# Performance work log

Hardware: AMD Instinct MI355X
Metric: run time of the kernel (lower is better)

Reference implementation:

```python
import jax, jax.numpy as jnp
import numpy as np

N, E = 50000, 200000
SIZES = [16, 32, 16]
EDIM = 8
EPS = 1e-5


def setup_inputs() -> dict:
    key = jax.random.key(0)
    ks = jax.random.split(key, 16)
    inp = {
        "x": jax.random.normal(ks[0], (N, SIZES[0]), jnp.float32),
        "edge_attr": jax.random.normal(ks[1], (E, EDIM), jnp.float32),
        "edge_index": jax.random.randint(ks[2], (2, E), 0, N, dtype=jnp.int32),
    }
    ki = 3
    for l in range(2):
        fin, fout = SIZES[l], SIZES[l + 1]
        m = fin * fout
        # xavier-ish init matching torch.nn.init.xavier_uniform_ scales
        inp[f"W1_{l}"] = jax.random.normal(ks[ki], (EDIM, m), jnp.float32) / np.float32(np.sqrt(EDIM)); ki += 1
        inp[f"b1_{l}"] = jnp.zeros((m,), jnp.float32)
        inp[f"W2_{l}"] = jax.random.normal(ks[ki], (m, m), jnp.float32) * np.float32(0.01 / np.sqrt(m)); ki += 1
        inp[f"b2_{l}"] = jnp.zeros((m,), jnp.float32)
        inp[f"root_{l}"] = jax.random.normal(ks[ki], (fin, fout), jnp.float32) / np.float32(np.sqrt(fin)); ki += 1
        inp[f"bias_{l}"] = jnp.zeros((fout,), jnp.float32)
        inp[f"gamma_{l}"] = jnp.ones((fout,), jnp.float32)
        inp[f"beta_{l}"] = jnp.zeros((fout,), jnp.float32)
    return inp


def _lrelu(v):
    return jnp.where(v >= 0, v, 0.01 * v)


def _nnconv(x, src, dst, edge_attr, W1, b1, W2, b2, root, bias, fin, fout):
    # edge MLP -> per-edge weight matrix [E, fin, fout]
    h = _lrelu(edge_attr @ W1 + b1) @ W2 + b2
    h = h.reshape(-1, fin, fout)
    # gather source node features, tiny per-edge matmul
    msg = jnp.einsum('ei,eio->eo', x[src], h)  # [E, fout]
    # scatter-mean aggregate at destination nodes
    agg = jax.ops.segment_sum(msg, dst, num_segments=N)
    deg = jax.ops.segment_sum(jnp.ones((msg.shape[0],), msg.dtype), dst, num_segments=N)
    agg = agg / jnp.maximum(deg, 1.0)[:, None]
    return agg + x @ root + bias


def _bn(v, gamma, beta):
    # BatchNorm1d (training mode: batch stats, biased variance)
    mu = v.mean(0)
    var = v.var(0)
    return (v - mu) * jax.lax.rsqrt(var + EPS) * gamma + beta


def reference(x, edge_attr,
              W1_0, b1_0, W2_0, b2_0, root_0, bias_0, gamma_0, beta_0,
              W1_1, b1_1, W2_1, b2_1, root_1, bias_1, gamma_1, beta_1,
              edge_index):
    src, dst = edge_index[0], edge_index[1]
    h = _nnconv(x, src, dst, edge_attr, W1_0, b1_0, W2_0, b2_0, root_0, bias_0, SIZES[0], SIZES[1])
    h = _lrelu(_bn(h, gamma_0, beta_0))
    h = _nnconv(h, src, dst, edge_attr, W1_1, b1_1, W2_1, b2_1, root_1, bias_1, SIZES[1], SIZES[2])
    return _bn(h, gamma_1, beta_1)
```

## Files before the change

### kernel.cpp

```cpp
#include <hip/hip_runtime.h>
#include <hip/hip_bf16.h>

typedef __attribute__((ext_vector_type(4))) float f32x4;
typedef __attribute__((ext_vector_type(8))) short s16x8;
typedef __attribute__((ext_vector_type(4))) int int4v;

#define DEVI __device__ __forceinline__

constexpr int NN = 50000;
constexpr int NE = 200000;
constexpr float BN_EPS = 1e-5f;

DEVI float bfbits2f(unsigned v) { union { unsigned u; float f; } t; t.u = v << 16; return t.f; }
DEVI float lrelu_f(float v) { return v >= 0.f ? v : 0.01f * v; }

__global__ void k_transpose_w2(const float* __restrict__ A0, const float* __restrict__ A1,
                               __hip_bfloat16* __restrict__ T0, __hip_bfloat16* __restrict__ T1) {
  const float* W2 = blockIdx.y ? A1 : A0;
  __hip_bfloat16* W2T = blockIdx.y ? T1 : T0;
  __shared__ float tile[32][33];
  int bx = blockIdx.x % 16, by = blockIdx.x / 16;
  int t = threadIdx.x;
  int r = t / 32, c = t % 32;
  for (int rr = r; rr < 32; rr += 8)
    tile[rr][c] = W2[(size_t)(by * 32 + rr) * 512 + bx * 32 + c];
  __syncthreads();
  for (int rr = r; rr < 32; rr += 8)
    W2T[(size_t)(bx * 32 + rr) * 512 + by * 32 + c] = __float2bfloat16(tile[c][rr]);
}

__global__ void k_transpose_w1(const float* __restrict__ A0, const float* __restrict__ A1,
                               __hip_bfloat16* __restrict__ T0, __hip_bfloat16* __restrict__ T1) {
  const float* W1 = blockIdx.y ? A1 : A0;
  __hip_bfloat16* W1T = blockIdx.y ? T1 : T0;
  int tid = blockIdx.x * 256 + threadIdx.x;
  if (tid < 8 * 512) {
    int k = tid / 512, n = tid % 512;
    W1T[n * 8 + k] = __float2bfloat16(W1[tid]);
  }
}

__global__ void k_count(const int* __restrict__ dst, int* __restrict__ cnt) {
  int e = blockIdx.x * 256 + threadIdx.x;
  if (e < NE) atomicAdd(&cnt[dst[e]], 1);
}

constexpr int SCAN_ELEMS = 1024;
__global__ void k_scan1(const int* __restrict__ cnt, int* __restrict__ base, int* __restrict__ aux, int n) {
  __shared__ int sw[256];
  int b = blockIdx.x, t = threadIdx.x;
  int i0 = b * SCAN_ELEMS + t * 4;
  int v[4]; int s = 0;
  #pragma unroll
  for (int j = 0; j < 4; j++) { int idx = i0 + j; v[j] = (idx < n) ? cnt[idx] : 0; s += v[j]; }
  sw[t] = s; __syncthreads();
  for (int d = 1; d < 256; d <<= 1) {
    int val = (t >= d) ? sw[t - d] : 0;
    __syncthreads();
    sw[t] += val;
    __syncthreads();
  }
  int run = (t > 0) ? sw[t - 1] : 0;
  #pragma unroll
  for (int j = 0; j < 4; j++) { int idx = i0 + j; if (idx < n) base[idx] = run; run += v[j]; }
  if (t == 255) aux[b] = sw[255];
}

__global__ void k_scan2(int* aux, int nb) {
  if (threadIdx.x == 0 && blockIdx.x == 0) {
    int run = 0;
    for (int i = 0; i < nb; i++) { int v = aux[i]; aux[i] = run; run += v; }
  }
}

__global__ void k_scan3(int* __restrict__ base, int* __restrict__ cursor, const int* __restrict__ aux, int n) {
  int i = blockIdx.x * 256 + threadIdx.x;
  if (i < n) { int v = base[i] + aux[i / SCAN_ELEMS]; base[i] = v; cursor[i] = v; }
}

__global__ void k_place(const int* __restrict__ dst, int* __restrict__ cursor, int* __restrict__ perm) {
  int e = blockIdx.x * 256 + threadIdx.x;
  if (e < NE) { int p = atomicAdd(&cursor[dst[e]], 1); perm[p] = e; }
}

template <int FIN, int FOUT>
__global__ __launch_bounds__(256, 3)
void k_edge(const float* __restrict__ x, const float* __restrict__ ea,
            const int* __restrict__ srcI,
            const __hip_bfloat16* __restrict__ W1T, const float* __restrict__ b1,
            const __hip_bfloat16* __restrict__ W2T, const float* __restrict__ b2,
            __hip_bfloat16* __restrict__ msgb)
{
  static_assert(FOUT == 32 || FOUT == 16, "");
  constexpr int TM = 256;
  constexpr int CG = 32;
  constexpr int NCGI = 16;
  constexpr int KH = 128;
  constexpr int NSW = 4;
  constexpr int NOT = FOUT / 16;
  constexpr int XLDS = TM + 8;

  __shared__ __align__(16) char bbuf[2][CG * 256];
  __shared__ __align__(16) char gbuf[4][4096];
  __shared__ __align__(16) __hip_bfloat16 xlt[FIN][XLDS];

  const int tid = threadIdx.x;
  const int lane = tid & 63, w = tid >> 6;
  const int l15 = lane & 15, l4 = lane >> 4;
  const int e0 = blockIdx.x * TM;
  const int rem = min(TM, NE - e0);
  const int wrow0 = w * 64;

  union { s16x8 v; int i4[4]; } earow;
  {
    int er = e0 + min(tid, rem - 1);
    float4 v0 = *(const float4*)(ea + (size_t)er * 8);
    float4 v1 = *(const float4*)(ea + (size_t)er * 8 + 4);
    __hip_bfloat16* p = (__hip_bfloat16*)&earow;
    p[0] = __float2bfloat16(v0.x); p[1] = __float2bfloat16(v0.y);
    p[2] = __float2bfloat16(v0.z); p[3] = __float2bfloat16(v0.w);
    p[4] = __float2bfloat16(v1.x); p[5] = __float2bfloat16(v1.y);
    p[6] = __float2bfloat16(v1.z); p[7] = __float2bfloat16(v1.w);
    int s = srcI[er];
    #pragma unroll
    for (int q = 0; q < FIN / 4; q++) {
      float4 xv4 = *(const float4*)(x + (size_t)s * FIN + q * 4);
      xlt[q * 4 + 0][tid] = __float2bfloat16(xv4.x);
      xlt[q * 4 + 1][tid] = __float2bfloat16(xv4.y);
      xlt[q * 4 + 2][tid] = __float2bfloat16(xv4.z);
      xlt[q * 4 + 3][tid] = __float2bfloat16(xv4.w);
    }
  }

  f32x4 msg[4][NOT];
  #pragma unroll
  for (int rt = 0; rt < 4; rt++)
    #pragma unroll
    for (int ot = 0; ot < NOT; ot++) msg[rt][ot] = (f32x4)(0.f);

  s16x8 af[4][4];
  const int st_col = tid >> 3, st_s = tid & 7;
  const char* W2Tb = (const char*)W2T;
  char* gme = gbuf[w];
  int4v sr0, sr1;

  for (int sw = 0; sw < NSW; ++sw) {
    {
      const char* gp = W2Tb + (size_t)st_col * 1024 + sw * 256;
      sr0 = *(const int4v*)(gp + st_s * 16);
      sr1 = *(const int4v*)(gp + (st_s + 8) * 16);
    }
    #pragma unroll
    for (int hr = 0; hr < 2; ++hr) {
      s16x8 afe[2];
      #pragma unroll
      for (int rt2 = 0; rt2 < 2; rt2++) {
        union { s16x8 v; int i4[4]; } t2;
        #pragma unroll
        for (int q = 0; q < 4; q++) t2.i4[q] = __shfl(earow.i4[q], (hr * 2 + rt2) * 16 + l15);
        afe[rt2] = (lane < 16) ? t2.v : (s16x8)0;
      }
      #pragma unroll
      for (int hk = 0; hk < 2; ++hk) {
        #pragma unroll
        for (int ct = 0; ct < 4; ct++) {
          int c = sw * KH + hk * 64 + ct * 16 + l15;
          s16x8 bw = *(const s16x8*)(W1T + c * 8);
          bw = (lane < 16) ? bw : (s16x8)0;
          float b1v = b1[c];
          #pragma unroll
          for (int rt2 = 0; rt2 < 2; rt2++) {
            f32x4 d = __builtin_amdgcn_mfma_f32_16x16x32_bf16(afe[rt2], bw, (f32x4)(0.f), 0, 0, 0);
            #pragma unroll
            for (int r = 0; r < 4; r++) {
              int rloc = rt2 * 16 + l4 * 4 + r;
              float gv = d[r] + b1v;
              gv = gv >= 0.f ? gv : 0.01f * gv;
              int byt = (rloc * 128 + (ct * 16 + l15) * 2) ^ ((rloc & 7) << 4);
              *(__hip_bfloat16*)(gme + byt) = __float2bfloat16(gv);
            }
          }
        }
        #pragma unroll
        for (int rt2 = 0; rt2 < 2; rt2++)
          #pragma unroll
          for (int kk = 0; kk < 2; kk++) {
            int rloc = rt2 * 16 + l15;
            int byt = (rloc * 128 + (kk * 32 + l4 * 8) * 2) ^ ((rloc & 7) << 4);
            af[hk * 2 + kk][hr * 2 + rt2] = *(const s16x8*)(gme + byt);
          }
      }
    }
    #pragma unroll
    for (int kst = 0; kst < 4; kst++)
      #pragma unroll
      for (int rt = 0; rt < 4; rt++)
        asm volatile("" : "+v"(af[kst][rt]));

    *(int4v*)(&bbuf[0][st_col * 256 + ((st_s ^ (st_col & 7)) << 4)]) = sr0;
    *(int4v*)(&bbuf[0][st_col * 256 + (((st_s + 8) ^ (st_col & 7)) << 4)]) = sr1;
    __syncthreads();

    for (int cgi = 0; cgi < NCGI; ++cgi) {
      if (cgi + 1 < NCGI) {
        const char* gp = W2Tb + (size_t)((cgi + 1) * CG + st_col) * 1024 + sw * 256;
        sr0 = *(const int4v*)(gp + st_s * 16);
        sr1 = *(const int4v*)(gp + (st_s + 8) * 16);
      }
      const char* bb = bbuf[cgi & 1];

      #pragma unroll
      for (int ct = 0; ct < 2; ++ct) {
        const int c = ct * 16 + l15;
        const int cbase = c * 256;
        const int csw = c & 7;
        f32x4 acc[4];
        if (sw == 0) {
          float b2v = b2[cgi * CG + c];
          acc[0] = (f32x4)(b2v); acc[1] = (f32x4)(b2v);
          acc[2] = (f32x4)(b2v); acc[3] = (f32x4)(b2v);
        } else {
          acc[0] = (f32x4)(0.f); acc[1] = (f32x4)(0.f);
          acc[2] = (f32x4)(0.f); acc[3] = (f32x4)(0.f);
        }
        #pragma unroll
        for (int kst = 0; kst < 4; ++kst) {
          const int slot = kst * 4 + l4;
          const s16x8 bw = *(const s16x8*)(bb + cbase + ((slot ^ csw) << 4));
          #pragma unroll
          for (int rt = 0; rt < 4; rt++)
            acc[rt] = __builtin_amdgcn_mfma_f32_16x16x32_bf16(af[kst][rt], bw, acc[rt], 0, 0, 0);
        }
        const int iv = (FOUT == 32) ? cgi : (cgi * 2 + ct);
        const int ot = (FOUT == 32) ? ct : 0;
        #pragma unroll
        for (int rt = 0; rt < 4; rt++) {
          int rbase = wrow0 + rt * 16 + l4 * 4;
          ushort4 xv = *(const ushort4*)(&xlt[iv][rbase]);
          msg[rt][ot][0] += bfbits2f(xv.x) * acc[rt][0];
          msg[rt][ot][1] += bfbits2f(xv.y) * acc[rt][1];
          msg[rt][ot][2] += bfbits2f(xv.z) * acc[rt][2];
          msg[rt][ot][3] += bfbits2f(xv.w) * acc[rt][3];
        }
      }
      if (cgi + 1 < NCGI) {
        char* bw2 = bbuf[(cgi + 1) & 1];
        *(int4v*)(&bw2[st_col * 256 + ((st_s ^ (st_col & 7)) << 4)]) = sr0;
        *(int4v*)(&bw2[st_col * 256 + (((st_s + 8) ^ (st_col & 7)) << 4)]) = sr1;
      }
      __syncthreads();
    }
  }

  #pragma unroll
  for (int rt = 0; rt < 4; rt++)
    #pragma unroll
    for (int r = 0; r < 4; r++) {
      int row = wrow0 + rt * 16 + l4 * 4 + r;
      if (row < rem) {
        #pragma unroll
        for (int ot = 0; ot < NOT; ot++)
          msgb[(size_t)(e0 + row) * FOUT + ot * 16 + l15] = __float2bfloat16(msg[rt][ot][r]);
      }
    }
}

template <int FIN, int FOUT>
__global__ void k_node_agg(const __hip_bfloat16* __restrict__ msgb, const int* __restrict__ perm,
                           const int* __restrict__ base,
                           const float* __restrict__ x,
                           const float* __restrict__ root,
                           const float* __restrict__ bias,
                           float* __restrict__ h)
{
  __shared__ float rl[FIN * FOUT];
  constexpr int NPB = 256 / FOUT;
  int t = threadIdx.x;
  for (int i = t; i < FIN * FOUT; i += 256) rl[i] = root[i];
  __syncthreads();
  int n = blockIdx.x * NPB + t / FOUT;
  int o = t % FOUT;
  if (n >= NN) return;
  int s = base[n];
  int e = (n + 1 < NN) ? base[n + 1] : NE;
  float sum = 0.f;
  for (int j = s; j < e; j++)
    sum += __bfloat162float(msgb[(size_t)perm[j] * FOUT + o]);
  float acc = sum / fmaxf((float)(e - s), 1.f) + bias[o];
  #pragma unroll
  for (int i = 0; i < FIN; i++)
    acc += x[(size_t)n * FIN + i] * rl[i * FOUT + o];
  h[(size_t)n * FOUT + o] = acc;
}

template <int FOUT>
__global__ void k_stats(const float* __restrict__ h, float* __restrict__ ssum, float* __restrict__ ssq) {
  constexpr int RPB = 256 / FOUT;
  int t = threadIdx.x;
  int o = t % FOUT, rr = t / FOUT;
  float v = 0.f, v2 = 0.f;
  for (int r = blockIdx.x * RPB + rr; r < NN; r += gridDim.x * RPB) {
    float y = h[(size_t)r * FOUT + o];
    v += y; v2 += y * y;
  }
  #pragma unroll
  for (int d = FOUT; d < 64; d <<= 1) { v += __shfl_xor(v, d); v2 += __shfl_xor(v2, d); }
  __shared__ float sv[4][32], sq[4][32];
  int wv = t >> 6, ln = t & 63;
  if (ln < FOUT) { sv[wv][ln] = v; sq[wv][ln] = v2; }
  __syncthreads();
  if (t < FOUT) {
    float a = 0.f, b = 0.f;
    #pragma unroll
    for (int w2 = 0; w2 < 4; w2++) { a += sv[w2][t]; b += sq[w2][t]; }
    atomicAdd(&ssum[t], a);
    atomicAdd(&ssq[t], b);
  }
}

template <int FOUT, bool LRELU>
__global__ void k_bn(const float* __restrict__ h, const float* __restrict__ ssum,
                     const float* __restrict__ ssq, const float* __restrict__ gamma,
                     const float* __restrict__ beta, float* __restrict__ out)
{
  int idx = blockIdx.x * 256 + threadIdx.x;
  if (idx * 4 >= NN * FOUT) return;
  float4 v = *(const float4*)(h + (size_t)idx * 4);
  float r[4] = {v.x, v.y, v.z, v.w};
  #pragma unroll
  for (int j = 0; j < 4; j++) {
    int o = (idx * 4 + j) % FOUT;
    float mu = ssum[o] * (1.f / NN);
    float var = ssq[o] * (1.f / NN) - mu * mu;
    float sc = rsqrtf(var + BN_EPS) * gamma[o];
    float y = (r[j] - mu) * sc + beta[o];
    if (LRELU) y = lrelu_f(y);
    r[j] = y;
  }
  *(float4*)(out + (size_t)idx * 4) = make_float4(r[0], r[1], r[2], r[3]);
}

extern "C" void kernel_launch(void* const* d_in, const int* in_sizes, int n_in,
                              void* d_out, int out_size, void* d_ws, size_t ws_size,
                              hipStream_t stream)
{
  const float* x0    = (const float*)d_in[0];
  const float* ea    = (const float*)d_in[1];
  const int*   ei    = (const int*)d_in[2];
  const float* W1_0  = (const float*)d_in[3];
  const float* b1_0  = (const float*)d_in[4];
  const float* W2_0  = (const float*)d_in[5];
  const float* b2_0  = (const float*)d_in[6];
  const float* root0 = (const float*)d_in[7];
  const float* bias0 = (const float*)d_in[8];
  const float* gam0  = (const float*)d_in[9];
  const float* bet0  = (const float*)d_in[10];
  const float* W1_1  = (const float*)d_in[11];
  const float* b1_1  = (const float*)d_in[12];
  const float* W2_1  = (const float*)d_in[13];
  const float* b2_1  = (const float*)d_in[14];
  const float* root1 = (const float*)d_in[15];
  const float* bias1 = (const float*)d_in[16];
  const float* gam1  = (const float*)d_in[17];
  const float* bet1  = (const float*)d_in[18];
  const int* srcI = ei;
  const int* dstI = ei + NE;

  char* ws = (char*)d_ws;
  size_t off = 0;
  auto alloc = [&](size_t bytes) { char* p = ws + off; off += (bytes + 255) & ~(size_t)255; return p; };
  int*   cnt   = (int*)alloc(50048 * 4);
  float* ssum0 = (float*)alloc(32 * 4);
  float* ssq0  = (float*)alloc(32 * 4);
  float* ssum1 = (float*)alloc(16 * 4);
  float* ssq1  = (float*)alloc(16 * 4);
  size_t zero_bytes = off;
  int*   base   = (int*)alloc(50048 * 4);
  int*   cursor = (int*)alloc(50048 * 4);
  int*   aux    = (int*)alloc(64 * 4);
  int*   perm   = (int*)alloc((size_t)NE * 4);
  __hip_bfloat16* msgb = (__hip_bfloat16*)alloc((size_t)NE * 32 * 2);
  float* h0 = (float*)alloc((size_t)NN * 32 * 4);
  float* h1 = (float*)alloc((size_t)NN * 16 * 4);
  float* x1 = (float*)alloc((size_t)NN * 32 * 4);
  __hip_bfloat16* W2T0 = (__hip_bfloat16*)alloc(512 * 512 * 2);
  __hip_bfloat16* W2T1 = (__hip_bfloat16*)alloc(512 * 512 * 2);
  __hip_bfloat16* W1T0 = (__hip_bfloat16*)alloc(512 * 8 * 2);
  __hip_bfloat16* W1T1 = (__hip_bfloat16*)alloc(512 * 8 * 2);

  hipMemsetAsync(d_ws, 0, zero_bytes, stream);

  k_transpose_w2<<<dim3(256, 2), 256, 0, stream>>>(W2_0, W2_1, W2T0, W2T1);
  k_transpose_w1<<<dim3(16, 2), 256, 0, stream>>>(W1_0, W1_1, W1T0, W1T1);

  constexpr int NSB = (NN + SCAN_ELEMS - 1) / SCAN_ELEMS;
  k_count<<<(NE + 255) / 256, 256, 0, stream>>>(dstI, cnt);
  k_scan1<<<NSB, 256, 0, stream>>>(cnt, base, aux, NN);
  k_scan2<<<1, 64, 0, stream>>>(aux, NSB);
  k_scan3<<<(NN + 255) / 256, 256, 0, stream>>>(base, cursor, aux, NN);
  k_place<<<(NE + 255) / 256, 256, 0, stream>>>(dstI, cursor, perm);

  constexpr int TM = 256;
  k_edge<16, 32><<<(NE + TM - 1) / TM, 256, 0, stream>>>(x0, ea, srcI, W1T0, b1_0, W2T0, b2_0, msgb);
  k_node_agg<16, 32><<<(NN + 7) / 8, 256, 0, stream>>>(msgb, perm, base, x0, root0, bias0, h0);
  k_stats<32><<<128, 256, 0, stream>>>(h0, ssum0, ssq0);
  k_bn<32, true><<<((NN * 32 / 4) + 255) / 256, 256, 0, stream>>>(h0, ssum0, ssq0, gam0, bet0, x1);

  k_edge<32, 16><<<(NE + TM - 1) / TM, 256, 0, stream>>>(x1, ea, srcI, W1T1, b1_1, W2T1, b2_1, msgb);
  k_node_agg<32, 16><<<(NN + 15) / 16, 256, 0, stream>>>(msgb, perm, base, x1, root1, bias1, h1);
  k_stats<16><<<128, 256, 0, stream>>>(h1, ssum1, ssq1);
  k_bn<16, false><<<((NN * 16 / 4) + 255) / 256, 256, 0, stream>>>(h1, ssum1, ssq1, gam1, bet1, (float*)d_out);
}
```

Baseline: 484.8 us.

## Stage whole W2 K-slice in LDS via direct global-to-LDS loads with 512-edge tiles

The edge kernel now processes 512 edges per 512-thread block and loads the entire per-sweep W2 K-slice (all 512 or 448 columns) into shared memory with global_load_lds, instead of double-buffering 32-column chunks through registers with a barrier per chunk. This removes the 16 per-chunk syncthreads per sweep and halves the number of W2 re-reads from L2. The tail columns that overlap the edge-MLP scratch are loaded after that stage and guarded by one extra barrier. For the FIN=32 layer, which has less LDS room, the last columns are read directly from global memory. The larger LDS footprint and block size may reduce occupancy, and the direct global reads in the tail may add latency.

```diff
diff --git a/kernel.cpp b/kernel.cpp
--- a/kernel.cpp
+++ b/kernel.cpp
@@ -6,6 +6,10 @@
 typedef __attribute__((ext_vector_type(4))) int int4v;
 
 #define DEVI __device__ __forceinline__
+
+#define GLL16(gp, lp) __builtin_amdgcn_global_load_lds( \
+    (const __attribute__((address_space(1))) void*)(gp), \
+    (__attribute__((address_space(3))) void*)(lp), 16, 0, 0)
 
 constexpr int NN = 50000;
 constexpr int NE = 200000;
@@ -84,7 +88,7 @@
 }
 
 template <int FIN, int FOUT>
-__global__ __launch_bounds__(256, 3)
+__global__ __launch_bounds__(512, 2)
 void k_edge(const float* __restrict__ x, const float* __restrict__ ea,
             const int* __restrict__ srcI,
             const __hip_bfloat16* __restrict__ W1T, const float* __restrict__ b1,
@@ -92,17 +96,19 @@
             __hip_bfloat16* __restrict__ msgb)
 {
   static_assert(FOUT == 32 || FOUT == 16, "");
-  constexpr int TM = 256;
-  constexpr int CG = 32;
-  constexpr int NCGI = 16;
-  constexpr int KH = 128;
-  constexpr int NSW = 4;
+  constexpr int TM = 512;
+  constexpr int KH = 128, NSW = 4;
   constexpr int NOT = FOUT / 16;
-  constexpr int XLDS = TM + 8;
-
-  __shared__ __align__(16) char bbuf[2][CG * 256];
-  __shared__ __align__(16) char gbuf[4][4096];
-  __shared__ __align__(16) __hip_bfloat16 xlt[FIN][XLDS];
+  constexpr int PCOLS = (FIN == 16) ? 512 : 448;
+  constexpr int NCGL = PCOLS / 32;
+  constexpr int CGC = (PCOLS - 128) / 32;
+  constexpr int MAINB = PCOLS * 256;
+  constexpr int GOFF = MAINB - 32768;
+  constexpr int NQE = (PCOLS - 128) / 4;
+  constexpr int QPW = NQE / 8;
+
+  __shared__ __align__(16) char main_[MAINB];
+  __shared__ __align__(16) __hip_bfloat16 xlt[FIN][TM];
 
   const int tid = threadIdx.x;
   const int lane = tid & 63, w = tid >> 6;
@@ -139,17 +145,19 @@
     for (int ot = 0; ot < NOT; ot++) msg[rt][ot] = (f32x4)(0.f);
 
   s16x8 af[4][4];
-  const int st_col = tid >> 3, st_s = tid & 7;
   const char* W2Tb = (const char*)W2T;
-  char* gme = gbuf[w];
-  int4v sr0, sr1;
+  char* gme = main_ + GOFF + w * 4096;
 
   for (int sw = 0; sw < NSW; ++sw) {
-    {
-      const char* gp = W2Tb + (size_t)st_col * 1024 + sw * 256;
-      sr0 = *(const int4v*)(gp + st_s * 16);
-      sr1 = *(const int4v*)(gp + (st_s + 8) * 16);
-    }
+    __syncthreads();
+    #pragma unroll
+    for (int t = 0; t < QPW; ++t) {
+      int colq = w * QPW + t;
+      int col = colq * 4 + (lane >> 4);
+      int ssrc = (lane & 15) ^ (col & 7);
+      GLL16(W2Tb + (size_t)col * 1024 + sw * 256 + (size_t)ssrc * 16, main_ + colq * 1024);
+    }
+
     #pragma unroll
     for (int hr = 0; hr < 2; ++hr) {
       s16x8 afe[2];
@@ -197,41 +205,34 @@
       for (int rt = 0; rt < 4; rt++)
         asm volatile("" : "+v"(af[kst][rt]));
 
-    *(int4v*)(&bbuf[0][st_col * 256 + ((st_s ^ (st_col & 7)) << 4)]) = sr0;
-    *(int4v*)(&bbuf[0][st_col * 256 + (((st_s + 8) ^ (st_col & 7)) << 4)]) = sr1;
     __syncthreads();
 
-    for (int cgi = 0; cgi < NCGI; ++cgi) {
-      if (cgi + 1 < NCGI) {
-        const char* gp = W2Tb + (size_t)((cgi + 1) * CG + st_col) * 1024 + sw * 256;
-        sr0 = *(const int4v*)(gp + st_s * 16);
-        sr1 = *(const int4v*)(gp + (st_s + 8) * 16);
-      }
-      const char* bb = bbuf[cgi & 1];
-
+    #pragma unroll
+    for (int t = 0; t < 4; ++t) {
+      int colq = NQE + w * 4 + t;
+      int col = colq * 4 + (lane >> 4);
+      int ssrc = (lane & 15) ^ (col & 7);
+      GLL16(W2Tb + (size_t)col * 1024 + sw * 256 + (size_t)ssrc * 16, main_ + colq * 1024);
+    }
+
+    for (int cgi = 0; cgi < NCGL; ++cgi) {
+      if (cgi == CGC) __syncthreads();
       #pragma unroll
       for (int ct = 0; ct < 2; ++ct) {
-        const int c = ct * 16 + l15;
-        const int cbase = c * 256;
-        const int csw = c & 7;
+        const int c = cgi * 32 + ct * 16 + l15;
         f32x4 acc[4];
-        if (sw == 0) {
-          float b2v = b2[cgi * CG + c];
-          acc[0] = (f32x4)(b2v); acc[1] = (f32x4)(b2v);
-          acc[2] = (f32x4)(b2v); acc[3] = (f32x4)(b2v);
-        } else {
-          acc[0] = (f32x4)(0.f); acc[1] = (f32x4)(0.f);
-          acc[2] = (f32x4)(0.f); acc[3] = (f32x4)(0.f);
-        }
+        float ai = (sw == 0) ? b2[c] : 0.f;
+        acc[0] = (f32x4)(ai); acc[1] = (f32x4)(ai);
+        acc[2] = (f32x4)(ai); acc[3] = (f32x4)(ai);
+        const int cbase = c * 256, csw = c & 7;
         #pragma unroll
         for (int kst = 0; kst < 4; ++kst) {
-          const int slot = kst * 4 + l4;
-          const s16x8 bw = *(const s16x8*)(bb + cbase + ((slot ^ csw) << 4));
+          const s16x8 bw = *(const s16x8*)(main_ + cbase + (((kst * 4 + l4) ^ csw) << 4));
           #pragma unroll
           for (int rt = 0; rt < 4; rt++)
             acc[rt] = __builtin_amdgcn_mfma_f32_16x16x32_bf16(af[kst][rt], bw, acc[rt], 0, 0, 0);
         }
-        const int iv = (FOUT == 32) ? cgi : (cgi * 2 + ct);
+        const int iv = (FOUT == 32) ? (c >> 5) : (c >> 4);
         const int ot = (FOUT == 32) ? ct : 0;
         #pragma unroll
         for (int rt = 0; rt < 4; rt++) {
@@ -243,12 +244,36 @@
           msg[rt][ot][3] += bfbits2f(xv.w) * acc[rt][3];
         }
       }
-      if (cgi + 1 < NCGI) {
-        char* bw2 = bbuf[(cgi + 1) & 1];
-        *(int4v*)(&bw2[st_col * 256 + ((st_s ^ (st_col & 7)) << 4)]) = sr0;
-        *(int4v*)(&bw2[st_col * 256 + (((st_s + 8) ^ (st_col & 7)) << 4)]) = sr1;
+    }
+    if constexpr (PCOLS < 512) {
+      for (int cgi = NCGL; cgi < 16; ++cgi) {
+        #pragma unroll
+        for (int ct = 0; ct < 2; ++ct) {
+          const int c = cgi * 32 + ct * 16 + l15;
+          f32x4 acc[4];
+          float ai = (sw == 0) ? b2[c] : 0.f;
+          acc[0] = (f32x4)(ai); acc[1] = (f32x4)(ai);
+          acc[2] = (f32x4)(ai); acc[3] = (f32x4)(ai);
+          #pragma unroll
+          for (int kst = 0; kst < 4; ++kst) {
+            const s16x8 bw = *(const s16x8*)(W2Tb + (size_t)c * 1024 + sw * 256 + (kst * 4 + l4) * 16);
+            #pragma unroll
+            for (int rt = 0; rt < 4; rt++)
+              acc[rt] = __builtin_amdgcn_mfma_f32_16x16x32_bf16(af[kst][rt], bw, acc[rt], 0, 0, 0);
+          }
+          const int iv = (FOUT == 32) ? (c >> 5) : (c >> 4);
+          const int ot = (FOUT == 32) ? ct : 0;
+          #pragma unroll
+          for (int rt = 0; rt < 4; rt++) {
+            int rbase = wrow0 + rt * 16 + l4 * 4;
+            ushort4 xv = *(const ushort4*)(&xlt[iv][rbase]);
+            msg[rt][ot][0] += bfbits2f(xv.x) * acc[rt][0];
+            msg[rt][ot][1] += bfbits2f(xv.y) * acc[rt][1];
+            msg[rt][ot][2] += bfbits2f(xv.z) * acc[rt][2];
+            msg[rt][ot][3] += bfbits2f(xv.w) * acc[rt][3];
+          }
+        }
       }
-      __syncthreads();
     }
   }
 
@@ -400,13 +425,13 @@
   k_scan3<<<(NN + 255) / 256, 256, 0, stream>>>(base, cursor, aux, NN);
   k_place<<<(NE + 255) / 256, 256, 0, stream>>>(dstI, cursor, perm);
 
-  constexpr int TM = 256;
-  k_edge<16, 32><<<(NE + TM - 1) / TM, 256, 0, stream>>>(x0, ea, srcI, W1T0, b1_0, W2T0, b2_0, msgb);
+  constexpr int TM = 512;
+  k_edge<16, 32><<<(NE + TM - 1) / TM, 512, 0, stream>>>(x0, ea, srcI, W1T0, b1_0, W2T0, b2_0, msgb);
   k_node_agg<16, 32><<<(NN + 7) / 8, 256, 0, stream>>>(msgb, perm, base, x0, root0, bias0, h0);
   k_stats<32><<<128, 256, 0, stream>>>(h0, ssum0, ssq0);
   k_bn<32, true><<<((NN * 32 / 4) + 255) / 256, 256, 0, stream>>>(h0, ssum0, ssq0, gam0, bet0, x1);
 
-  k_edge<32, 16><<<(NE + TM - 1) / TM, 256, 0, stream>>>(x1, ea, srcI, W1T1, b1_1, W2T1, b2_1, msgb);
+  k_edge<32, 16><<<(NE + TM - 1) / TM, 512, 0, stream>>>(x1, ea, srcI, W1T1, b1_1, W2T1, b2_1, msgb);
   k_node_agg<32, 16><<<(NN + 15) / 16, 256, 0, stream>>>(msgb, perm, base, x1, root1, bias1, h1);
   k_stats<16><<<128, 256, 0, stream>>>(h1, ssum1, ssq1);
   k_bn<16, false><<<((NN * 16 / 4) + 255) / 256, 256, 0, stream>>>(h1, ssum1, ssq1, gam1, bet1, (float*)d_out);
```

Measured after the change: 455.4 us. 1.06x faster.

## Switch edge kernel to 32x32x16 MFMA with 512-edge tiles and 256-wide K chunks

Applied to the files above, without the earlier changes.

Rewrites the per-edge MLP kernel to use 32x32x16 bf16 MFMA tiles instead of 16x16x32, doubles the edge tile to 512 with 512-thread blocks, and halves the number of K sweeps over W2 by staging 256-wide chunks. The aim is to raise MFMA efficiency per shared-memory B-fragment load and to reload W2 fewer times per edge. In exchange it holds many more A fragments in registers (16x2 s16x8), which raises register pressure and may cut occupancy. It also adds a shuffle reduction for the FOUT=16 output.

```diff
diff --git a/kernel.cpp b/kernel.cpp
--- a/kernel.cpp
+++ b/kernel.cpp
@@ -2,6 +2,7 @@
 #include <hip/hip_bf16.h>
 
 typedef __attribute__((ext_vector_type(4))) float f32x4;
+typedef __attribute__((ext_vector_type(16))) float f32x16;
 typedef __attribute__((ext_vector_type(8))) short s16x8;
 typedef __attribute__((ext_vector_type(4))) int int4v;
 
@@ -84,7 +85,7 @@
 }
 
 template <int FIN, int FOUT>
-__global__ __launch_bounds__(256, 3)
+__global__ __launch_bounds__(512, 2)
 void k_edge(const float* __restrict__ x, const float* __restrict__ ea,
             const int* __restrict__ srcI,
             const __hip_bfloat16* __restrict__ W1T, const float* __restrict__ b1,
@@ -92,21 +93,20 @@
             __hip_bfloat16* __restrict__ msgb)
 {
   static_assert(FOUT == 32 || FOUT == 16, "");
-  constexpr int TM = 256;
+  constexpr int TM = 512;
   constexpr int CG = 32;
   constexpr int NCGI = 16;
-  constexpr int KH = 128;
-  constexpr int NSW = 4;
-  constexpr int NOT = FOUT / 16;
+  constexpr int KH = 256;
+  constexpr int NSW = 2;
   constexpr int XLDS = TM + 8;
 
-  __shared__ __align__(16) char bbuf[2][CG * 256];
-  __shared__ __align__(16) char gbuf[4][4096];
+  __shared__ __align__(16) char bbuf[2][CG * 512];
+  __shared__ __align__(16) char gbuf[8][4096];
   __shared__ __align__(16) __hip_bfloat16 xlt[FIN][XLDS];
 
   const int tid = threadIdx.x;
   const int lane = tid & 63, w = tid >> 6;
-  const int l15 = lane & 15, l4 = lane >> 4;
+  const int l31 = lane & 31, lhi = lane >> 5;
   const int e0 = blockIdx.x * TM;
   const int rem = min(TM, NE - e0);
   const int wrow0 = w * 64;
@@ -132,137 +132,131 @@
     }
   }
 
-  f32x4 msg[4][NOT];
-  #pragma unroll
-  for (int rt = 0; rt < 4; rt++)
-    #pragma unroll
-    for (int ot = 0; ot < NOT; ot++) msg[rt][ot] = (f32x4)(0.f);
-
-  s16x8 af[4][4];
-  const int st_col = tid >> 3, st_s = tid & 7;
+  f32x16 msg0 = (f32x16)(0.f), msg1 = (f32x16)(0.f);
+  s16x8 af[16][2];
+  const int st_col = tid >> 4, st_s = tid & 15;
   const char* W2Tb = (const char*)W2T;
   char* gme = gbuf[w];
   int4v sr0, sr1;
 
   for (int sw = 0; sw < NSW; ++sw) {
     {
-      const char* gp = W2Tb + (size_t)st_col * 1024 + sw * 256;
+      const char* gp = W2Tb + (size_t)st_col * 1024 + sw * 512;
       sr0 = *(const int4v*)(gp + st_s * 16);
-      sr1 = *(const int4v*)(gp + (st_s + 8) * 16);
-    }
-    #pragma unroll
-    for (int hr = 0; hr < 2; ++hr) {
-      s16x8 afe[2];
-      #pragma unroll
-      for (int rt2 = 0; rt2 < 2; rt2++) {
+      sr1 = *(const int4v*)(gp + (st_s + 16) * 16);
+    }
+    #pragma unroll
+    for (int tile = 0; tile < 2; ++tile) {
+      s16x8 ae;
+      {
         union { s16x8 v; int i4[4]; } t2;
         #pragma unroll
-        for (int q = 0; q < 4; q++) t2.i4[q] = __shfl(earow.i4[q], (hr * 2 + rt2) * 16 + l15);
-        afe[rt2] = (lane < 16) ? t2.v : (s16x8)0;
-      }
-      #pragma unroll
-      for (int hk = 0; hk < 2; ++hk) {
+        for (int q = 0; q < 4; q++) t2.i4[q] = __shfl(earow.i4[q], tile * 32 + l31);
+        ae = (lane < 32) ? t2.v : (s16x8)0;
+      }
+      #pragma unroll
+      for (int chunk = 0; chunk < 4; ++chunk) {
         #pragma unroll
-        for (int ct = 0; ct < 4; ct++) {
-          int c = sw * KH + hk * 64 + ct * 16 + l15;
-          s16x8 bw = *(const s16x8*)(W1T + c * 8);
-          bw = (lane < 16) ? bw : (s16x8)0;
-          float b1v = b1[c];
+        for (int ctile = 0; ctile < 2; ++ctile) {
+          int gcolg = sw * KH + chunk * 64 + ctile * 32 + l31;
+          s16x8 bw = (s16x8)0;
+          if (lane < 32) bw = *(const s16x8*)(W1T + gcolg * 8);
+          float b1v = b1[gcolg];
+          f32x16 d = __builtin_amdgcn_mfma_f32_32x32x16_bf16(ae, bw, (f32x16)(0.f), 0, 0, 0);
           #pragma unroll
-          for (int rt2 = 0; rt2 < 2; rt2++) {
-            f32x4 d = __builtin_amdgcn_mfma_f32_16x16x32_bf16(afe[rt2], bw, (f32x4)(0.f), 0, 0, 0);
-            #pragma unroll
-            for (int r = 0; r < 4; r++) {
-              int rloc = rt2 * 16 + l4 * 4 + r;
-              float gv = d[r] + b1v;
-              gv = gv >= 0.f ? gv : 0.01f * gv;
-              int byt = (rloc * 128 + (ct * 16 + l15) * 2) ^ ((rloc & 7) << 4);
-              *(__hip_bfloat16*)(gme + byt) = __float2bfloat16(gv);
-            }
+          for (int r = 0; r < 16; r++) {
+            int rowloc = (r & 3) + 8 * (r >> 2) + 4 * lhi;
+            float gv = d[r] + b1v;
+            gv = gv >= 0.f ? gv : 0.01f * gv;
+            int gcl = ctile * 32 + l31;
+            int byt = (rowloc * 128 + gcl * 2) ^ ((rowloc & 7) << 4);
+            *(__hip_bfloat16*)(gme + byt) = __float2bfloat16(gv);
           }
         }
         #pragma unroll
-        for (int rt2 = 0; rt2 < 2; rt2++)
-          #pragma unroll
-          for (int kk = 0; kk < 2; kk++) {
-            int rloc = rt2 * 16 + l15;
-            int byt = (rloc * 128 + (kk * 32 + l4 * 8) * 2) ^ ((rloc & 7) << 4);
-            af[hk * 2 + kk][hr * 2 + rt2] = *(const s16x8*)(gme + byt);
-          }
-      }
-    }
-    #pragma unroll
-    for (int kst = 0; kst < 4; kst++)
-      #pragma unroll
-      for (int rt = 0; rt < 4; rt++)
-        asm volatile("" : "+v"(af[kst][rt]));
-
-    *(int4v*)(&bbuf[0][st_col * 256 + ((st_s ^ (st_col & 7)) << 4)]) = sr0;
-    *(int4v*)(&bbuf[0][st_col * 256 + (((st_s + 8) ^ (st_col & 7)) << 4)]) = sr1;
+        for (int kk = 0; kk < 4; ++kk) {
+          int byt = (l31 * 128 + (kk * 16 + lhi * 8) * 2) ^ ((l31 & 7) << 4);
+          af[chunk * 4 + kk][tile] = *(const s16x8*)(gme + byt);
+        }
+      }
+    }
+    #pragma unroll
+    for (int kst = 0; kst < 16; kst++)
+      #pragma unroll
+      for (int tile = 0; tile < 2; tile++)
+        asm volatile("" : "+v"(af[kst][tile]));
+
+    *(int4v*)(&bbuf[0][st_col * 512 + ((st_s ^ (st_col & 7)) << 4)]) = sr0;
+    *(int4v*)(&bbuf[0][st_col * 512 + (((st_s + 16) ^ (st_col & 7)) << 4)]) = sr1;
     __syncthreads();
 
     for (int cgi = 0; cgi < NCGI; ++cgi) {
       if (cgi + 1 < NCGI) {
-        const char* gp = W2Tb + (size_t)((cgi + 1) * CG + st_col) * 1024 + sw * 256;
+        const char* gp = W2Tb + (size_t)((cgi + 1) * CG + st_col) * 1024 + sw * 512;
         sr0 = *(const int4v*)(gp + st_s * 16);
-        sr1 = *(const int4v*)(gp + (st_s + 8) * 16);
+        sr1 = *(const int4v*)(gp + (st_s + 16) * 16);
       }
       const char* bb = bbuf[cgi & 1];
-
-      #pragma unroll
-      for (int ct = 0; ct < 2; ++ct) {
-        const int c = ct * 16 + l15;
-        const int cbase = c * 256;
-        const int csw = c & 7;
-        f32x4 acc[4];
-        if (sw == 0) {
-          float b2v = b2[cgi * CG + c];
-          acc[0] = (f32x4)(b2v); acc[1] = (f32x4)(b2v);
-          acc[2] = (f32x4)(b2v); acc[3] = (f32x4)(b2v);
-        } else {
-          acc[0] = (f32x4)(0.f); acc[1] = (f32x4)(0.f);
-          acc[2] = (f32x4)(0.f); acc[3] = (f32x4)(0.f);
-        }
-        #pragma unroll
-        for (int kst = 0; kst < 4; ++kst) {
-          const int slot = kst * 4 + l4;
-          const s16x8 bw = *(const s16x8*)(bb + cbase + ((slot ^ csw) << 4));
-          #pragma unroll
-          for (int rt = 0; rt < 4; rt++)
-            acc[rt] = __builtin_amdgcn_mfma_f32_16x16x32_bf16(af[kst][rt], bw, acc[rt], 0, 0, 0);
-        }
-        const int iv = (FOUT == 32) ? cgi : (cgi * 2 + ct);
-        const int ot = (FOUT == 32) ? ct : 0;
-        #pragma unroll
-        for (int rt = 0; rt < 4; rt++) {
-          int rbase = wrow0 + rt * 16 + l4 * 4;
-          ushort4 xv = *(const ushort4*)(&xlt[iv][rbase]);
-          msg[rt][ot][0] += bfbits2f(xv.x) * acc[rt][0];
-          msg[rt][ot][1] += bfbits2f(xv.y) * acc[rt][1];
-          msg[rt][ot][2] += bfbits2f(xv.z) * acc[rt][2];
-          msg[rt][ot][3] += bfbits2f(xv.w) * acc[rt][3];
-        }
+      float ai = (sw == 0) ? b2[cgi * CG + l31] : 0.f;
+      f32x16 a0 = (f32x16)(ai), a1 = (f32x16)(ai);
+
+      #pragma unroll
+      for (int kst = 0; kst < 16; ++kst) {
+        const int slot = kst * 2 + lhi;
+        const s16x8 bw = *(const s16x8*)(bb + l31 * 512 + ((slot ^ (l31 & 7)) << 4));
+        a0 = __builtin_amdgcn_mfma_f32_32x32x16_bf16(af[kst][0], bw, a0, 0, 0, 0);
+        a1 = __builtin_amdgcn_mfma_f32_32x32x16_bf16(af[kst][1], bw, a1, 0, 0, 0);
+      }
+
+      const int iv = (FOUT == 32) ? cgi : (cgi * 2 + ((lane >> 4) & 1));
+      #pragma unroll
+      for (int q = 0; q < 4; ++q) {
+        int rb0 = wrow0 + q * 8 + 4 * lhi;
+        ushort4 xv0 = *(const ushort4*)(&xlt[iv][rb0]);
+        msg0[q * 4 + 0] += bfbits2f(xv0.x) * a0[q * 4 + 0];
+        msg0[q * 4 + 1] += bfbits2f(xv0.y) * a0[q * 4 + 1];
+        msg0[q * 4 + 2] += bfbits2f(xv0.z) * a0[q * 4 + 2];
+        msg0[q * 4 + 3] += bfbits2f(xv0.w) * a0[q * 4 + 3];
+        ushort4 xv1 = *(const ushort4*)(&xlt[iv][rb0 + 32]);
+        msg1[q * 4 + 0] += bfbits2f(xv1.x) * a1[q * 4 + 0];
+        msg1[q * 4 + 1] += bfbits2f(xv1.y) * a1[q * 4 + 1];
+        msg1[q * 4 + 2] += bfbits2f(xv1.z) * a1[q * 4 + 2];
+        msg1[q * 4 + 3] += bfbits2f(xv1.w) * a1[q * 4 + 3];
       }
       if (cgi + 1 < NCGI) {
         char* bw2 = bbuf[(cgi + 1) & 1];
-        *(int4v*)(&bw2[st_col * 256 + ((st_s ^ (st_col & 7)) << 4)]) = sr0;
-        *(int4v*)(&bw2[st_col * 256 + (((st_s + 8) ^ (st_col & 7)) << 4)]) = sr1;
+        *(int4v*)(&bw2[st_col * 512 + ((st_s ^ (st_col & 7)) << 4)]) = sr0;
+        *(int4v*)(&bw2[st_col * 512 + (((st_s + 16) ^ (st_col & 7)) << 4)]) = sr1;
       }
       __syncthreads();
     }
   }
 
-  #pragma unroll
-  for (int rt = 0; rt < 4; rt++)
-    #pragma unroll
-    for (int r = 0; r < 4; r++) {
-      int row = wrow0 + rt * 16 + l4 * 4 + r;
-      if (row < rem) {
-        #pragma unroll
-        for (int ot = 0; ot < NOT; ot++)
-          msgb[(size_t)(e0 + row) * FOUT + ot * 16 + l15] = __float2bfloat16(msg[rt][ot][r]);
-      }
-    }
+  if constexpr (FOUT == 32) {
+    #pragma unroll
+    for (int tile = 0; tile < 2; ++tile) {
+      const f32x16& mg = tile ? msg1 : msg0;
+      #pragma unroll
+      for (int r = 0; r < 16; r++) {
+        int row = wrow0 + tile * 32 + (r & 3) + 8 * (r >> 2) + 4 * lhi;
+        if (row < rem)
+          msgb[(size_t)(e0 + row) * 32 + l31] = __float2bfloat16(mg[r]);
+      }
+    }
+  } else {
+    #pragma unroll
+    for (int tile = 0; tile < 2; ++tile) {
+      const f32x16& mg = tile ? msg1 : msg0;
+      #pragma unroll
+      for (int r = 0; r < 16; r++) {
+        float v = mg[r];
+        v += __shfl_xor(v, 16);
+        int row = wrow0 + tile * 32 + (r & 3) + 8 * (r >> 2) + 4 * lhi;
+        if (!(lane & 16) && row < rem)
+          msgb[(size_t)(e0 + row) * 16 + (lane & 15)] = __float2bfloat16(v);
+      }
+    }
+  }
 }
 
 template <int FIN, int FOUT>
@@ -400,13 +394,13 @@
   k_scan3<<<(NN + 255) / 256, 256, 0, stream>>>(base, cursor, aux, NN);
   k_place<<<(NE + 255) / 256, 256, 0, stream>>>(dstI, cursor, perm);
 
-  constexpr int TM = 256;
-  k_edge<16, 32><<<(NE + TM - 1) / TM, 256, 0, stream>>>(x0, ea, srcI, W1T0, b1_0, W2T0, b2_0, msgb);
+  constexpr int TM = 512;
+  k_edge<16, 32><<<(NE + TM - 1) / TM, 512, 0, stream>>>(x0, ea, srcI, W1T0, b1_0, W2T0, b2_0, msgb);
   k_node_agg<16, 32><<<(NN + 7) / 8, 256, 0, stream>>>(msgb, perm, base, x0, root0, bias0, h0);
   k_stats<32><<<128, 256, 0, stream>>>(h0, ssum0, ssq0);
   k_bn<32, true><<<((NN * 32 / 4) + 255) / 256, 256, 0, stream>>>(h0, ssum0, ssq0, gam0, bet0, x1);
 
-  k_edge<32, 16><<<(NE + TM - 1) / TM, 256, 0, stream>>>(x1, ea, srcI, W1T1, b1_1, W2T1, b2_1, msgb);
+  k_edge<32, 16><<<(NE + TM - 1) / TM, 512, 0, stream>>>(x1, ea, srcI, W1T1, b1_1, W2T1, b2_1, msgb);
   k_node_agg<32, 16><<<(NN + 15) / 16, 256, 0, stream>>>(msgb, perm, base, x1, root1, bias1, h1);
   k_stats<16><<<128, 256, 0, stream>>>(h1, ssum1, ssq1);
   k_bn<16, false><<<((NN * 16 / 4) + 255) / 256, 256, 0, stream>>>(h1, ssum1, ssq1, gam1, bet1, (float*)d_out);
```

Result: faster. 435.1 us (-10.2%).
